# Performance work log

Measured on AMD Instinct MI355X. Metric: run time of the kernel, lower is better.

Reference implementation:

```python
import jax, jax.numpy as jnp
import numpy as np
from jax.scipy.special import logsumexp

B, S, D, L = 64, 512, 1024, 9


def setup_inputs() -> dict:
    key = jax.random.key(0)
    k1, k2, k3, k4, k5, k6 = jax.random.split(key, 6)
    inputs = jax.random.normal(k1, (B, S, D), dtype=jnp.float32)
    targets = jax.random.randint(k2, (B, S), 0, L)
    sequence_lengths = jax.random.randint(k3, (B,), S // 2, S + 1)
    mask = (jnp.arange(S)[None, :] < sequence_lengths[:, None])
    W = jax.random.normal(k4, (D, L), dtype=jnp.float32) * (1.0 / np.sqrt(D))
    b = jnp.zeros((L,), dtype=jnp.float32)
    transitions = jax.random.normal(k5, (L, L), dtype=jnp.float32) * 0.1
    return {"inputs": inputs, "targets": targets, "sequence_lengths": sequence_lengths,
            "mask": mask, "W": W, "b": b, "transitions": transitions}


def crf_nll(logits, tags, mask, transitions):
    # logits: [B,S,L], tags: [B,S] int, mask: [B,S] bool, transitions: [L,L]
    maskf = mask.astype(logits.dtype)
    # gold-path score (numerator)
    emit = jnp.take_along_axis(logits, tags[..., None], axis=2)[..., 0]  # [B,S]
    trans = transitions[tags[:, :-1], tags[:, 1:]]                        # [B,S-1]
    numerator = (emit * maskf).sum(-1) + (trans * maskf[:, 1:]).sum(-1)   # [B]
    # partition function via forward algorithm (scan over time)
    alpha0 = logits[:, 0]  # [B,L]; position 0 always valid
    emit_t = jnp.swapaxes(logits[:, 1:], 0, 1)   # [S-1,B,L]
    mask_t = jnp.swapaxes(mask[:, 1:], 0, 1)     # [S-1,B]

    def step(alpha, xs):
        e, m = xs
        scores = alpha[:, :, None] + transitions[None, :, :] + e[:, None, :]  # [B,L,L]
        new = logsumexp(scores, axis=1)                                        # [B,L]
        alpha = jnp.where(m[:, None], new, alpha)
        return alpha, None

    alpha, _ = jax.lax.scan(step, alpha0, (emit_t, mask_t))
    denominator = logsumexp(alpha, axis=-1)  # [B]
    return -(numerator - denominator).sum()


def reference(inputs, targets, sequence_lengths, mask, W, b, transitions):
    logits = jnp.einsum('bsd,dl->bsl', inputs, W) + b  # nn.Linear
    values = crf_nll(logits, targets, mask, transitions)
    return (values, logits)
```

## Files before the change

kernel.cpp:

```cpp
#include <hip/hip_runtime.h>
#include <hip/hip_bf16.h>
#include <math.h>

#define BB 64
#define SS 512
#define DD 1024
#define LL 9
#define NCHUNK 32

#define DPP_ADD(v, ctrl)                                                     \
  v += __int_as_float(__builtin_amdgcn_update_dpp(                           \
      0, __float_as_int(v), ctrl, 0xF, 0xF, false))

template <int R>
__device__ inline float swz(float x) {
  return __int_as_float(
      __builtin_amdgcn_ds_swizzle(__float_as_int(x), (R << 10) | 0x1F));
}

__global__ __launch_bounds__(256) void fused_kernel(
    const float* __restrict__ in, const float* __restrict__ W,
    const float* __restrict__ bias, const int* __restrict__ targets,
    const int* __restrict__ seqlen, const float* __restrict__ trans,
    float* __restrict__ logits, float* __restrict__ mats,
    float* __restrict__ scales, float* __restrict__ numblk,
    unsigned* __restrict__ counter) {
  __shared__ float Wt[LL][DD];
  __shared__ float Lg[64][LL];
  int tid = threadIdx.x;
  int bid = blockIdx.x;
  if (bid == 0 && tid == 0) *counter = 0u;

  for (int i = tid; i < DD * LL; i += 256) {
    int k = i / LL, l = i - k * LL;
    Wt[l][k] = W[i];
  }
  __syncthreads();

  int lane = tid & 63;
  int wave = tid >> 6;
  int p = lane & 15;
  int sub = lane >> 4;

  int r0 = bid * 64 + wave * 16 + sub;
  const float* x0 = in + (size_t)r0 * DD + p * 4;

  float acc[4][LL];
#pragma unroll
  for (int q = 0; q < 4; ++q)
#pragma unroll
    for (int l = 0; l < LL; ++l) acc[q][l] = 0.f;

  float4 a[4], an[4];
#pragma unroll
  for (int q = 0; q < 4; ++q)
    a[q] = *reinterpret_cast<const float4*>(x0 + (size_t)q * 4 * DD);

  for (int it = 0; it < 16; ++it) {
    if (it < 15) {
#pragma unroll
      for (int q = 0; q < 4; ++q)
        an[q] = *reinterpret_cast<const float4*>(x0 + (size_t)q * 4 * DD +
                                                 (it + 1) * 64);
    }
    int k0 = it * 64 + p * 4;
    float4 w4[LL];
#pragma unroll
    for (int l = 0; l < LL; ++l)
      w4[l] = *reinterpret_cast<const float4*>(&Wt[l][k0]);
#pragma unroll
    for (int q = 0; q < 4; ++q)
#pragma unroll
      for (int l = 0; l < LL; ++l)
        acc[q][l] += a[q].x * w4[l].x + a[q].y * w4[l].y + a[q].z * w4[l].z +
                     a[q].w * w4[l].w;
    if (it < 15) {
#pragma unroll
      for (int q = 0; q < 4; ++q) a[q] = an[q];
    }
  }

#pragma unroll
  for (int q = 0; q < 4; ++q)
#pragma unroll
    for (int l = 0; l < LL; ++l) {
      DPP_ADD(acc[q][l], 0x111);
      DPP_ADD(acc[q][l], 0x112);
      DPP_ADD(acc[q][l], 0x114);
      DPP_ADD(acc[q][l], 0x118);
    }
  if (p == 15) {
#pragma unroll
    for (int q = 0; q < 4; ++q)
#pragma unroll
      for (int l = 0; l < LL; ++l) {
        float v = acc[q][l] + bias[l];
        logits[(size_t)(r0 + q * 4) * LL + l] = v;
        Lg[wave * 16 + sub + q * 4][l] = v;
      }
  }
  __syncthreads();

  int b = bid >> 3;
  int base = (bid & 7) * 64;
  int len = seqlen[b];

  if (wave == 0) {
    int j = lane & 15;
    int g = lane >> 4;
    int kk = (bid & 7) * 4 + g;
    int gid = b * NCHUNK + kk;

    float Mx[81];
#pragma unroll
    for (int i = 0; i < 81; ++i) Mx[i] = __expf(trans[i]);

    float T[LL];
#pragma unroll
    for (int c = 0; c < LL; ++c) T[c] = (j == c) ? 1.f : 0.f;
    float Cl = 0.f;

    int tstart = (kk == 0) ? 1 : kk * 16;
    int tend = kk * 16 + 16;

    float e[LL];
#pragma unroll
    for (int c = 0; c < LL; ++c) e[c] = Lg[tstart - base][c];

    for (int t = tstart; t < tend; ++t) {
      float Ex[LL];
#pragma unroll
      for (int c = 0; c < LL; ++c) Ex[c] = __expf(e[c]);
      if (t + 1 < tend) {
#pragma unroll
        for (int c = 0; c < LL; ++c) e[c] = Lg[t + 1 - base][c];
      }
      bool active = (t < len);
      float nT[LL];
#pragma unroll
      for (int c = 0; c < LL; ++c) {
        float s = 0.f;
#pragma unroll
        for (int m = 0; m < LL; ++m) s += T[m] * Mx[m * LL + c];
        nT[c] = s * Ex[c];
      }
#pragma unroll
      for (int c = 0; c < LL; ++c) T[c] = active ? nT[c] : T[c];

      if (((t - tstart) & 7) == 7) {
        float m = T[0];
#pragma unroll
        for (int c = 1; c < LL; ++c) m = fmaxf(m, T[c]);
        m = fmaxf(m, swz<1>(m));
        m = fmaxf(m, swz<2>(m));
        m = fmaxf(m, swz<4>(m));
        m = fmaxf(m, swz<8>(m));
        float inv = 1.f / m;
#pragma unroll
        for (int c = 0; c < LL; ++c) T[c] *= inv;
        Cl += __logf(m);
      }
    }
    {
      float m = T[0];
#pragma unroll
      for (int c = 1; c < LL; ++c) m = fmaxf(m, T[c]);
      m = fmaxf(m, swz<1>(m));
      m = fmaxf(m, swz<2>(m));
      m = fmaxf(m, swz<4>(m));
      m = fmaxf(m, swz<8>(m));
      float inv = 1.f / m;
#pragma unroll
      for (int c = 0; c < LL; ++c) T[c] *= inv;
      Cl += __logf(m);
    }

    float* Mg = mats + (size_t)gid * 256;
#pragma unroll
    for (int c = 0; c < 16; ++c)
      Mg[c * 16 + (j ^ c)] = (c < LL) ? T[c] : 0.f;
    if (j == 0) scales[gid] = Cl;
  } else if (wave == 1) {
    int t = base + lane;
    float np = 0.f;
    const int* tb = targets + (size_t)b * SS;
    if (t >= 1 && t < len) {
      int tg = tb[t];
      np = Lg[lane][tg] + trans[tb[t - 1] * LL + tg];
    }
    np += __shfl_xor(np, 1, 64);
    np += __shfl_xor(np, 2, 64);
    np += __shfl_xor(np, 4, 64);
    np += __shfl_xor(np, 8, 64);
    np += __shfl_xor(np, 16, 64);
    np += __shfl_xor(np, 32, 64);
    if (lane == 0) numblk[bid] = np;
  }
}

__global__ __launch_bounds__(64) void crf_combine_kernel(
    const float* __restrict__ logits, const int* __restrict__ targets,
    const float* __restrict__ mats, const float* __restrict__ scales,
    const float* __restrict__ numblk, float* __restrict__ partials,
    unsigned* __restrict__ counter, float* __restrict__ out_val) {
  int lane = threadIdx.x;
  int j = lane & 15;
  int b = blockIdx.x;
  const float* lb = logits + (size_t)b * SS * LL;
  const float* Mb = mats + (size_t)b * NCHUNK * 256;

  float extra = 0.f;
  if (lane < NCHUNK) extra = scales[b * NCHUNK + lane];
  else if (lane < NCHUNK + 8) extra = -numblk[b * 8 + (lane - NCHUNK)];
  extra += __shfl_xor(extra, 1, 64);
  extra += __shfl_xor(extra, 2, 64);
  extra += __shfl_xor(extra, 4, 64);
  extra += __shfl_xor(extra, 8, 64);
  extra += __shfl_xor(extra, 16, 64);
  extra += __shfl_xor(extra, 32, 64);
  float emit0 = lb[targets[(size_t)b * SS]];

  float alpha = (j < LL) ? __expf(lb[j]) : 0.f;
  float C = 0.f;

  float4 c0 = *reinterpret_cast<const float4*>(Mb + j * 16 + 0);
  float4 c1 = *reinterpret_cast<const float4*>(Mb + j * 16 + 4);
  float4 c2 = *reinterpret_cast<const float4*>(Mb + j * 16 + 8);
  float4 c3 = *reinterpret_cast<const float4*>(Mb + j * 16 + 12);

  for (int k = 0; k < NCHUNK; ++k) {
    float4 n0, n1, n2, n3;
    if (k + 1 < NCHUNK) {
      const float* Mn = Mb + (size_t)(k + 1) * 256 + j * 16;
      n0 = *reinterpret_cast<const float4*>(Mn + 0);
      n1 = *reinterpret_cast<const float4*>(Mn + 4);
      n2 = *reinterpret_cast<const float4*>(Mn + 8);
      n3 = *reinterpret_cast<const float4*>(Mn + 12);
    }
    float s01 = alpha * c0.x + swz<1>(alpha) * c0.y;
    float s23 = swz<2>(alpha) * c0.z + swz<3>(alpha) * c0.w;
    float s45 = swz<4>(alpha) * c1.x + swz<5>(alpha) * c1.y;
    float s67 = swz<6>(alpha) * c1.z + swz<7>(alpha) * c1.w;
    float s89 = swz<8>(alpha) * c2.x + swz<9>(alpha) * c2.y;
    float sab = swz<10>(alpha) * c2.z + swz<11>(alpha) * c2.w;
    float scd = swz<12>(alpha) * c3.x + swz<13>(alpha) * c3.y;
    float sef = swz<14>(alpha) * c3.z + swz<15>(alpha) * c3.w;
    alpha = ((s01 + s23) + (s45 + s67)) + ((s89 + sab) + (scd + sef));

    if ((k & 3) == 3) {
      float m = alpha;
      m = fmaxf(m, swz<1>(m));
      m = fmaxf(m, swz<2>(m));
      m = fmaxf(m, swz<4>(m));
      m = fmaxf(m, swz<8>(m));
      float inv = 1.f / m;
      alpha *= inv;
      C += __logf(m);
    }
    if (k + 1 < NCHUNK) { c0 = n0; c1 = n1; c2 = n2; c3 = n3; }
  }

  float s = alpha;
  s += swz<1>(s);
  s += swz<2>(s);
  s += swz<4>(s);
  s += swz<8>(s);
  float result = extra + C + __logf(s) - emit0;

  if (lane == 0) partials[b] = result;
  __threadfence();
  unsigned old = 0;
  if (lane == 0) old = atomicAdd(counter, 1u);
  old = __shfl(old, 0, 64);
  if (old == BB - 1) {
    __threadfence();
    float v = partials[lane];
    v += __shfl_xor(v, 1, 64);
    v += __shfl_xor(v, 2, 64);
    v += __shfl_xor(v, 4, 64);
    v += __shfl_xor(v, 8, 64);
    v += __shfl_xor(v, 16, 64);
    v += __shfl_xor(v, 32, 64);
    if (lane == 0) {
      out_val[0] = v;
      *counter = 0u;
    }
  }
}

extern "C" void kernel_launch(void* const* d_in, const int* in_sizes, int n_in,
                              void* d_out, int out_size, void* d_ws,
                              size_t ws_size, hipStream_t stream) {
  const float* inputs = (const float*)d_in[0];
  const int* targets = (const int*)d_in[1];
  const int* seqlen = (const int*)d_in[2];
  const float* W = (const float*)d_in[4];
  const float* bias = (const float*)d_in[5];
  const float* trans = (const float*)d_in[6];
  float* out = (float*)d_out;

  float* mats = (float*)d_ws;
  float* scales = mats + (size_t)BB * NCHUNK * 256;
  float* numblk = scales + (size_t)BB * NCHUNK;
  float* partials = numblk + 512;
  unsigned* counter = (unsigned*)(partials + BB);

  fused_kernel<<<512, 256, 0, stream>>>(inputs, W, bias, targets, seqlen,
                                        trans, out + 1, mats, scales, numblk,
                                        counter);
  crf_combine_kernel<<<BB, 64, 0, stream>>>(out + 1, targets, mats, scales,
                                            numblk, partials, counter, out);
}
```

Before: 52.96 us.

## Restructure GEMV so each wave processes two full rows per step with wave-wide reduction

The projection loop is reorganized so that all 64 lanes of a wave split one row's 1024-wide dot product, handling two rows at a time and prefetching the next pair, instead of 16 lanes per row across four rows. Row sums now use a full 64-lane DPP reduction (adding row-broadcast steps), and the bias is hoisted into registers. Launch bounds also request two blocks per CU to lower register pressure and raise occupancy. The trade-off is many more cross-lane reduction instructions per row, which replace the shorter 16-lane reduction.

```diff
diff --git a/kernel.cpp b/kernel.cpp
--- a/kernel.cpp
+++ b/kernel.cpp
@@ -11,6 +11,15 @@
 #define DPP_ADD(v, ctrl)                                                     \
   v += __int_as_float(__builtin_amdgcn_update_dpp(                           \
       0, __float_as_int(v), ctrl, 0xF, 0xF, false))
+#define WAVE_RED63(v)                                                        \
+  do {                                                                       \
+    DPP_ADD(v, 0x111);                                                       \
+    DPP_ADD(v, 0x112);                                                       \
+    DPP_ADD(v, 0x114);                                                       \
+    DPP_ADD(v, 0x118);                                                       \
+    DPP_ADD(v, 0x142);                                                       \
+    DPP_ADD(v, 0x143);                                                       \
+  } while (0)
 
 template <int R>
 __device__ inline float swz(float x) {
@@ -18,7 +27,7 @@
       __builtin_amdgcn_ds_swizzle(__float_as_int(x), (R << 10) | 0x1F));
 }
 
-__global__ __launch_bounds__(256) void fused_kernel(
+__global__ __launch_bounds__(256, 2) void fused_kernel(
     const float* __restrict__ in, const float* __restrict__ W,
     const float* __restrict__ bias, const int* __restrict__ targets,
     const int* __restrict__ seqlen, const float* __restrict__ trans,
@@ -39,65 +48,74 @@
 
   int lane = tid & 63;
   int wave = tid >> 6;
-  int p = lane & 15;
-  int sub = lane >> 4;
-
-  int r0 = bid * 64 + wave * 16 + sub;
-  const float* x0 = in + (size_t)r0 * DD + p * 4;
-
-  float acc[4][LL];
-#pragma unroll
-  for (int q = 0; q < 4; ++q)
-#pragma unroll
-    for (int l = 0; l < LL; ++l) acc[q][l] = 0.f;
-
-  float4 a[4], an[4];
-#pragma unroll
-  for (int q = 0; q < 4; ++q)
-    a[q] = *reinterpret_cast<const float4*>(x0 + (size_t)q * 4 * DD);
-
-  for (int it = 0; it < 16; ++it) {
-    if (it < 15) {
-#pragma unroll
-      for (int q = 0; q < 4; ++q)
-        an[q] = *reinterpret_cast<const float4*>(x0 + (size_t)q * 4 * DD +
-                                                 (it + 1) * 64);
-    }
-    int k0 = it * 64 + p * 4;
-    float4 w4[LL];
-#pragma unroll
-    for (int l = 0; l < LL; ++l)
-      w4[l] = *reinterpret_cast<const float4*>(&Wt[l][k0]);
-#pragma unroll
-    for (int q = 0; q < 4; ++q)
+
+  float bv[LL];
+#pragma unroll
+  for (int l = 0; l < LL; ++l) bv[l] = bias[l];
+
+  int rbase = bid * 64 + wave * 16;
+
+  float4 a[8], an[8];
+  {
+    const float* src = in + (size_t)rbase * DD + lane * 4;
+#pragma unroll
+    for (int j = 0; j < 8; ++j)
+      a[j] = *reinterpret_cast<const float4*>(src + (size_t)(j >> 2) * DD +
+                                              (j & 3) * 256);
+  }
+
+  for (int t = 0; t < 8; ++t) {
+    int r = rbase + 2 * t;
+    if (t < 7) {
+      const float* src = in + (size_t)(r + 2) * DD + lane * 4;
+#pragma unroll
+      for (int j = 0; j < 8; ++j)
+        an[j] = *reinterpret_cast<const float4*>(src + (size_t)(j >> 2) * DD +
+                                                 (j & 3) * 256);
+    }
+    float acc0[LL], acc1[LL];
+#pragma unroll
+    for (int l = 0; l < LL; ++l) { acc0[l] = 0.f; acc1[l] = 0.f; }
+
+#pragma unroll
+    for (int i = 0; i < 4; ++i) {
+      float4 w4[LL];
 #pragma unroll
       for (int l = 0; l < LL; ++l)
-        acc[q][l] += a[q].x * w4[l].x + a[q].y * w4[l].y + a[q].z * w4[l].z +
-                     a[q].w * w4[l].w;
-    if (it < 15) {
-#pragma unroll
-      for (int q = 0; q < 4; ++q) a[q] = an[q];
-    }
-  }
-
-#pragma unroll
-  for (int q = 0; q < 4; ++q)
+        w4[l] = *reinterpret_cast<const float4*>(&Wt[l][i * 256 + lane * 4]);
+      float4 x0 = a[i];
+      float4 x1 = a[4 + i];
+#pragma unroll
+      for (int l = 0; l < LL; ++l) {
+        acc0[l] += x0.x * w4[l].x + x0.y * w4[l].y + x0.z * w4[l].z +
+                   x0.w * w4[l].w;
+        acc1[l] += x1.x * w4[l].x + x1.y * w4[l].y + x1.z * w4[l].z +
+                   x1.w * w4[l].w;
+      }
+    }
+
 #pragma unroll
     for (int l = 0; l < LL; ++l) {
-      DPP_ADD(acc[q][l], 0x111);
-      DPP_ADD(acc[q][l], 0x112);
-      DPP_ADD(acc[q][l], 0x114);
-      DPP_ADD(acc[q][l], 0x118);
-    }
-  if (p == 15) {
-#pragma unroll
-    for (int q = 0; q < 4; ++q)
+      WAVE_RED63(acc0[l]);
+      WAVE_RED63(acc1[l]);
+    }
+    if (lane == 63) {
+      int lr = r - bid * 64;
+      float* g0 = logits + (size_t)r * LL;
 #pragma unroll
       for (int l = 0; l < LL; ++l) {
-        float v = acc[q][l] + bias[l];
-        logits[(size_t)(r0 + q * 4) * LL + l] = v;
-        Lg[wave * 16 + sub + q * 4][l] = v;
-      }
+        float v0 = acc0[l] + bv[l];
+        float v1 = acc1[l] + bv[l];
+        g0[l] = v0;
+        g0[LL + l] = v1;
+        Lg[lr][l] = v0;
+        Lg[lr + 1][l] = v1;
+      }
+    }
+    if (t < 7) {
+#pragma unroll
+      for (int j = 0; j < 8; ++j) a[j] = an[j];
+    }
   }
   __syncthreads();
 
```

Result: slower. 191.2 us (+261.0%).
